# Kernel tuning notes

Measured on AMD Instinct MI355X. Metric: run time of the kernel, lower is better.

The kernel has to match this reference:

```python
import jax, jax.numpy as jnp
import numpy as np
import math

B, N, H = 2, 2048, 16
D_NOPE, D_ROPE, D_V = 128, 64, 128
Q_HEAD_DIM = D_NOPE + D_ROPE  # 192
HID, QR, KVR = 2048, 1536, 512
THETA = 10000.0
EPS = 1e-6


def _rmsnorm(x, w):
    var = jnp.mean(jnp.square(x.astype(jnp.float32)), axis=-1, keepdims=True)
    return w * (x * jax.lax.rsqrt(var + EPS)).astype(x.dtype)


def _permute_pairs(x):
    # torch: view(..., d//2, 2).transpose(-1,-2).reshape(..., d)
    # -> concat(evens, odds) along last dim
    return jnp.concatenate([x[..., 0::2], x[..., 1::2]], axis=-1)


def _rotate_half(x):
    x1, x2 = x[..., : x.shape[-1] // 2], x[..., x.shape[-1] // 2:]
    return jnp.concatenate([-x2, x1], axis=-1)


def _rope_tables(pos_ids):
    inv_freq = 1.0 / (THETA ** (jnp.arange(0, D_ROPE, 2, dtype=jnp.float32) / D_ROPE))
    t = jnp.arange(N, dtype=jnp.float32)
    freqs = jnp.outer(t, inv_freq)                 # [N, 32]
    emb = jnp.concatenate([freqs, freqs], axis=-1) # [N, 64]
    cos = jnp.cos(emb)[pos_ids][:, None]           # [B, 1, N, 64]
    sin = jnp.sin(emb)[pos_ids][:, None]
    return cos, sin


def mla_forward(x, Wq_down, q_norm_w, Wq_up, Wkv_down, kv_norm_w, Wkv_up, Wo, mask, pos_ids):
    b, n, _ = x.shape
    # low-rank Q path
    q = _rmsnorm(x @ Wq_down, q_norm_w) @ Wq_up          # [B, N, H*192]
    q = q.reshape(b, n, H, Q_HEAD_DIM).transpose(0, 2, 1, 3)  # [B, H, N, 192]
    q_nope, q_pe = q[..., :D_NOPE], q[..., D_NOPE:]
    # low-rank KV path
    kv = x @ Wkv_down                                    # [B, N, 512+64]
    kv_c, k_pe = kv[..., :KVR], kv[..., KVR:]
    k_pe = k_pe.reshape(b, n, 1, D_ROPE).transpose(0, 2, 1, 3)  # [B, 1, N, 64]
    kv_up = _rmsnorm(kv_c, kv_norm_w) @ Wkv_up           # [B, N, H*256]
    kv_up = kv_up.reshape(b, n, H, D_NOPE + D_V).transpose(0, 2, 1, 3)  # [B, H, N, 256]
    k_nope, v = kv_up[..., :D_NOPE], kv_up[..., D_NOPE:]
    # partial RoPE (with the pair-permute quirk from the torch code)
    cos, sin = _rope_tables(pos_ids)
    q_pe = _permute_pairs(q_pe)
    k_pe = _permute_pairs(k_pe)
    q_pe = q_pe * cos + _rotate_half(q_pe) * sin
    k_pe = k_pe * cos + _rotate_half(k_pe) * sin
    q_full = jnp.concatenate([q_nope, q_pe], axis=-1)                       # [B, H, N, 192]
    k_full = jnp.concatenate([k_nope, jnp.broadcast_to(k_pe, (b, H, n, D_ROPE))], axis=-1)
    scores = jnp.einsum('bhqd,bhkd->bhqk', q_full, k_full) / math.sqrt(Q_HEAD_DIM)
    scores = jnp.where(mask == 0, -jnp.inf, scores)
    attn = jax.nn.softmax(scores.astype(jnp.float32), axis=-1)
    out = jnp.einsum('bhqk,bhkd->bhqd', attn, v)          # [B, H, N, 128]
    out = out.transpose(0, 2, 1, 3).reshape(b, n, H * D_V)
    return out @ Wo


def setup_inputs() -> dict:
    key = jax.random.key(0)
    ks = jax.random.split(key, 7)
    s = 0.02
    return {
        'x': jax.random.normal(ks[0], (B, N, HID), jnp.float32),
        'Wq_down': jax.random.normal(ks[1], (HID, QR), jnp.float32) * s,
        'q_norm_w': jnp.ones((QR,), jnp.float32),
        'Wq_up': jax.random.normal(ks[2], (QR, H * Q_HEAD_DIM), jnp.float32) * s,
        'Wkv_down': jax.random.normal(ks[3], (HID, KVR + D_ROPE), jnp.float32) * s,
        'kv_norm_w': jnp.ones((KVR,), jnp.float32),
        'Wkv_up': jax.random.normal(ks[4], (KVR, H * (D_NOPE + D_V)), jnp.float32) * s,
        'Wo': jax.random.normal(ks[5], (H * D_V, HID), jnp.float32) * s,
        'mask': jnp.ones((1, 1, N, N), jnp.bool_),
        'pos_ids': jnp.broadcast_to(jnp.arange(N, dtype=jnp.int32), (B, N)),
    }


def reference(x, Wq_down, q_norm_w, Wq_up, Wkv_down, kv_norm_w, Wkv_up, Wo, mask, pos_ids):
    return mla_forward(x, Wq_down, q_norm_w, Wq_up, Wkv_down, kv_norm_w, Wkv_up, Wo, mask, pos_ids)
```

## Files before the change

kernel.cpp:

```cpp
#include <hip/hip_runtime.h>
#include <hip/hip_bf16.h>
#include <cstdint>

#define B_ 2
#define N_ 2048
#define H_ 16
#define HID_ 2048
#define QR_ 1536
#define KVR_ 512
#define DN_ 128
#define DR_ 64
#define DV_ 128
#define QHD_ 192

typedef __attribute__((ext_vector_type(8))) short short8;
typedef __attribute__((ext_vector_type(4))) float f32x4;

union bfu { __hip_bfloat16 b; short s; };

static __device__ __forceinline__ void bf_split(float v, short& hi, short& lo) {
  bfu uh, ul;
  uh.b = __float2bfloat16(v);
  float hf = __bfloat162float(uh.b);
  ul.b = __float2bfloat16(v - hf);
  hi = uh.s; lo = ul.s;
}

static __device__ __forceinline__ void gload16(const void* g, void* l) {
  __builtin_amdgcn_global_load_lds(
      (const __attribute__((address_space(1))) uint32_t*)(g),
      (__attribute__((address_space(3))) uint32_t*)(l), 16, 0, 0);
}


__global__ __launch_bounds__(256) void conv_a_kernel(
    const float* __restrict__ A, uint8_t* __restrict__ img, int K, int nks, int total) {
  int gid = blockIdx.x * 256 + threadIdx.x;
  if (gid >= total) return;
  int perRow = K >> 3;
  int row = gid / perRow, kc = (gid - row * perRow) << 3;
  const float* src = A + (size_t)row * K + kc;
  short8 hi, lo;
#pragma unroll
  for (int j = 0; j < 8; ++j) { short a, b; bf_split(src[j], a, b); hi[j] = a; lo[j] = b; }
  int mb = row >> 7, r = row & 127, sw = (r & 7) << 4;
  uint8_t* base = img + ((size_t)mb * nks << 14) + r * 128;
  auto put = [&](int p, short8 v) {
    int ks = p >> 6, s = (p >> 3) & 7;
    *(short8*)(base + ((size_t)ks << 14) + ((16 * s) ^ sw)) = v;
  };
  put(kc, hi); put(K + kc, lo); put(2 * K + kc, hi);
}

__global__ __launch_bounds__(256) void conv_b_kernel(
    const float* __restrict__ Bw, uint8_t* __restrict__ img, int K, int N,
    int Npad, int nbase, int nks, int total) {
  int gid = blockIdx.x * 256 + threadIdx.x;
  if (gid >= total) return;
  int perN = K >> 3;
  int n = gid / perN, kc = (gid - n * perN) << 3;
  short8 hi = {0,0,0,0,0,0,0,0}, lo = {0,0,0,0,0,0,0,0};
  if (n < N) {
#pragma unroll
    for (int j = 0; j < 8; ++j) {
      short a, b; bf_split(Bw[(size_t)(kc + j) * N + n], a, b); hi[j] = a; lo[j] = b;
    }
  }
  int nn = nbase * 128 + n;
  int nb = nn >> 7, r = nn & 127, sw = (r & 7) << 4;
  uint8_t* base = img + ((size_t)nb * nks << 14) + r * 128;
  auto put = [&](int p, short8 v) {
    int ks = p >> 6, s = (p >> 3) & 7;
    *(short8*)(base + ((size_t)ks << 14) + ((16 * s) ^ sw)) = v;
  };
  put(kc, hi); put(K + kc, hi); put(2 * K + kc, lo);
}

__global__ __launch_bounds__(256) void rmsnorm_img_kernel(
    const float* __restrict__ in, const float* __restrict__ w,
    uint8_t* __restrict__ img, int len, int istride, int nks) {
  __shared__ float red[4];
  const int row = blockIdx.x;
  const float* x = in + (size_t)row * istride;
  float ss = 0.f;
  for (int i = threadIdx.x; i < len; i += 256) { float v = x[i]; ss += v * v; }
#pragma unroll
  for (int o = 32; o > 0; o >>= 1) ss += __shfl_down(ss, o, 64);
  if ((threadIdx.x & 63) == 0) red[threadIdx.x >> 6] = ss;
  __syncthreads();
  if (threadIdx.x == 0)
    red[0] = rsqrtf((red[0] + red[1] + red[2] + red[3]) / (float)len + 1e-6f);
  __syncthreads();
  const float inv = red[0];
  int mb = row >> 7, r = row & 127, sw = (r & 7) << 4;
  uint8_t* base = img + ((size_t)mb * nks << 14) + r * 128;
  auto put = [&](int p, short8 v) {
    int ks = p >> 6, s = (p >> 3) & 7;
    *(short8*)(base + ((size_t)ks << 14) + ((16 * s) ^ sw)) = v;
  };
  for (int kc = threadIdx.x * 8; kc < len; kc += 2048) {
    short8 hi, lo;
#pragma unroll
    for (int j = 0; j < 8; ++j) {
      short a, b; bf_split(w[kc + j] * (x[kc + j] * inv), a, b); hi[j] = a; lo[j] = b;
    }
    put(kc, hi); put(len + kc, lo); put(2 * len + kc, hi);
  }
}

template <int MODE>
__global__ __launch_bounds__(256) void gemm_bf16_kernel(
    const uint8_t* __restrict__ Aimg, const uint8_t* __restrict__ Bimg,
    float* __restrict__ C, int N, int nks,
    uint8_t* __restrict__ Kn, uint8_t* __restrict__ Vv) {
  __shared__ __align__(16) uint8_t As[16384];
  __shared__ __align__(16) uint8_t Bs[16384];
  const int tid = threadIdx.x;
  const int lane = tid & 63;
  const int wave = tid >> 6;
  const int wm = wave >> 1, wn = wave & 1;
  const int lr = lane & 15, g = lane >> 4;
  const int mb = blockIdx.y, nb = blockIdx.x;
  const uint8_t* ga = Aimg + ((size_t)mb * nks << 14);
  const uint8_t* gb = Bimg + ((size_t)nb * nks << 14);

  f32x4 acc[4][4];
#pragma unroll
  for (int i = 0; i < 4; ++i)
#pragma unroll
    for (int j = 0; j < 4; ++j) acc[i][j] = (f32x4){0.f, 0.f, 0.f, 0.f};

  for (int ks = 0; ks < nks; ++ks) {
    __syncthreads();
#pragma unroll
    for (int i = 0; i < 4; ++i)
      gload16(ga + ((size_t)ks << 14) + (wave * 4 + i) * 1024 + lane * 16,
              As + (wave * 4 + i) * 1024);
#pragma unroll
    for (int i = 0; i < 4; ++i)
      gload16(gb + ((size_t)ks << 14) + (wave * 4 + i) * 1024 + lane * 16,
              Bs + (wave * 4 + i) * 1024);
    __syncthreads();
#pragma unroll
    for (int c = 0; c < 2; ++c) {
      short8 af[4], bf[4];
#pragma unroll
      for (int i = 0; i < 4; ++i) {
        int ar = wm * 64 + i * 16 + lr;
        af[i] = *(const short8*)(As + ar * 128 + ((16 * (c * 4 + g)) ^ ((ar & 7) << 4)));
        int br = wn * 64 + i * 16 + lr;
        bf[i] = *(const short8*)(Bs + br * 128 + ((16 * (c * 4 + g)) ^ ((br & 7) << 4)));
      }
#pragma unroll
      for (int i = 0; i < 4; ++i)
#pragma unroll
        for (int j = 0; j < 4; ++j)
          acc[i][j] = __builtin_amdgcn_mfma_f32_16x16x32_bf16(af[i], bf[j], acc[i][j], 0, 0, 0);
    }
  }

  if (MODE == 0) {
#pragma unroll
    for (int i = 0; i < 4; ++i)
#pragma unroll
      for (int q = 0; q < 4; ++q) {
        float* rp = C + (size_t)(mb * 128 + wm * 64 + i * 16 + g * 4 + q) * N +
                    nb * 128 + wn * 64 + lr;
#pragma unroll
        for (int j = 0; j < 4; ++j) rp[j * 16] = acc[i][j][q];
      }
  } else {
#pragma unroll
    for (int i = 0; i < 4; ++i)
#pragma unroll
      for (int j = 0; j < 4; ++j)
#pragma unroll
        for (int q = 0; q < 4; ++q) {
          int trow = mb * 128 + wm * 64 + i * 16 + g * 4 + q;
          int nn = nb * 128 + wn * 64 + j * 16 + lr;
          int h = nn >> 8, half = (nn >> 7) & 1, d = nn & 127;
          int b = trow >> 11, t = trow & 2047, kt = t >> 5, r = t & 31;
          int bh = b * 16 + h;
          short hi, lo; bf_split(acc[i][j][q], hi, lo);
          if (half == 0) {
            uint8_t* tp = Kn + (((size_t)bh * 64 + kt) << 14) + r * 512;
            int sw = (r & 7) << 4, s = d >> 3;
            *(short*)(tp + ((16 * s) ^ sw) + (d & 7) * 2) = hi;
            *(short*)(tp + ((16 * (s + 16)) ^ sw) + (d & 7) * 2) = lo;
          } else {
            uint8_t* tp = Vv + (((size_t)bh * 64 + kt) << 14) + d * 128;
            int sw = (d & 7) << 4, gg = r >> 3;
            *(short*)(tp + ((16 * gg) ^ sw) + (r & 7) * 2) = hi;
            *(short*)(tp + ((16 * (gg + 4)) ^ sw) + (r & 7) * 2) = lo;
          }
        }
  }
}

__device__ __forceinline__ void rope_apply(const float* __restrict__ src,
                                           float* __restrict__ dst, float pos) {
  float xv[64];
#pragma unroll
  for (int i = 0; i < 64; ++i) xv[i] = src[i];
#pragma unroll
  for (int i = 0; i < 32; ++i) {
    float freq = __expf(-0.2878231366f * (float)i);
    float s, c;
    sincosf(pos * freq, &s, &c);
    dst[i]      = xv[2 * i] * c - xv[2 * i + 1] * s;
    dst[i + 32] = xv[2 * i + 1] * c + xv[2 * i] * s;
  }
}

__global__ __launch_bounds__(256) void rope_q_kernel(float* __restrict__ q,
                                                     const int* __restrict__ pos_ids) {
  int idx = blockIdx.x * 256 + threadIdx.x;
  if (idx >= B_ * N_ * H_) return;
  int t = idx >> 4, h = idx & 15;
  float* p = q + (size_t)t * (H_ * QHD_) + h * QHD_ + DN_;
  rope_apply(p, p, (float)pos_ids[t]);
}

__global__ __launch_bounds__(256) void rope_k_kernel(const float* __restrict__ Cmat,
                                                     const int* __restrict__ pos_ids,
                                                     uint8_t* __restrict__ Kp) {
  int t = blockIdx.x * 256 + threadIdx.x;
  if (t >= B_ * N_) return;
  float rv[64];
  rope_apply(Cmat + (size_t)t * 2176 + 2048, rv, (float)pos_ids[t]);
  int b = t >> 11, tt = t & 2047, kt = tt >> 5, r = tt & 31;
  uint8_t* tp = Kp + (((size_t)b * 64 + kt) << 13) + r * 256;
  int sw = (r & 7) << 4;
#pragma unroll
  for (int s = 0; s < 8; ++s) {
    short8 hi, lo;
#pragma unroll
    for (int j = 0; j < 8; ++j) { short a, bq; bf_split(rv[s * 8 + j], a, bq); hi[j] = a; lo[j] = bq; }
    *(short8*)(tp + ((16 * s) ^ sw)) = hi;
    *(short8*)(tp + ((16 * (s + 8)) ^ sw)) = lo;
  }
}

__global__ __launch_bounds__(256, 3) void attn_mfma_kernel(
    const float* __restrict__ q_up,
    const uint8_t* __restrict__ Kn, const uint8_t* __restrict__ Kp,
    const uint8_t* __restrict__ Vv,
    float* __restrict__ aout) {
  __shared__ __align__(16) uint8_t Ksn[32 * 512];
  __shared__ __align__(16) uint8_t Ksp[32 * 256];
  __shared__ __align__(16) uint8_t Vs[128 * 128];
  __shared__ __align__(16) uint8_t Ps[4 * 2048];

  const int tid = threadIdx.x;
  const int lane = tid & 63;
  const int wave = tid >> 6;
  const int g = lane >> 4;
  const int lr = lane & 15;
  const int bh = blockIdx.y;
  const int b = bh >> 4, h = bh & 15;
  const int q0 = blockIdx.x << 6;

  short8 qhi[6], qlo[6];
  {
    const int tok = b * N_ + q0 + wave * 16 + lr;
    const float* qp = q_up + (size_t)tok * (H_ * QHD_) + h * QHD_;
    const float scale = 0.07216878364870323f;
#pragma unroll
    for (int c = 0; c < 6; ++c) {
      const float* src = qp + c * 32 + g * 8;
#pragma unroll
      for (int j = 0; j < 8; ++j) {
        short a, bq; bf_split(src[j] * scale, a, bq);
        qhi[c][j] = a; qlo[c][j] = bq;
      }
    }
  }

  f32x4 acc_o[8];
#pragma unroll
  for (int i = 0; i < 8; ++i) acc_o[i] = (f32x4){0.f, 0.f, 0.f, 0.f};
  float m_r[4], l_r[4];
#pragma unroll
  for (int j = 0; j < 4; ++j) { m_r[j] = -1e30f; l_r[j] = 0.f; }

  for (int kt = 0; kt < N_ / 32; ++kt) {
    __syncthreads();
    {
      const uint8_t* gkn = Kn + (((size_t)bh * 64 + kt) << 14);
      const uint8_t* gkp = Kp + (((size_t)b * 64 + kt) << 13);
      const uint8_t* gv  = Vv + (((size_t)bh * 64 + kt) << 14);
#pragma unroll
      for (int i = 0; i < 4; ++i)
        gload16(gkn + (wave * 4 + i) * 1024 + lane * 16, Ksn + (wave * 4 + i) * 1024);
#pragma unroll
      for (int i = 0; i < 2; ++i)
        gload16(gkp + (wave * 2 + i) * 1024 + lane * 16, Ksp + (wave * 2 + i) * 1024);
#pragma unroll
      for (int i = 0; i < 4; ++i)
        gload16(gv + (wave * 4 + i) * 1024 + lane * 16, Vs + (wave * 4 + i) * 1024);
    }
    __syncthreads();

    f32x4 accs[2];
#pragma unroll
    for (int t = 0; t < 2; ++t) {
      f32x4 a = {0.f, 0.f, 0.f, 0.f};
      const int krow = t * 16 + lr;
      const int sw = (krow & 7) << 4;
      const uint8_t* kb = Ksn + krow * 512;
#pragma unroll
      for (int c = 0; c < 4; ++c) {
        short8 kh = *(const short8*)(kb + ((16 * (c * 4 + g)) ^ sw));
        short8 kl = *(const short8*)(kb + ((16 * (c * 4 + g + 16)) ^ sw));
        a = __builtin_amdgcn_mfma_f32_16x16x32_bf16(qhi[c], kh, a, 0, 0, 0);
        a = __builtin_amdgcn_mfma_f32_16x16x32_bf16(qhi[c], kl, a, 0, 0, 0);
        a = __builtin_amdgcn_mfma_f32_16x16x32_bf16(qlo[c], kh, a, 0, 0, 0);
      }
      const uint8_t* pb = Ksp + krow * 256;
#pragma unroll
      for (int c2 = 0; c2 < 2; ++c2) {
        short8 kh = *(const short8*)(pb + ((16 * (c2 * 4 + g)) ^ sw));
        short8 kl = *(const short8*)(pb + ((16 * (c2 * 4 + g + 8)) ^ sw));
        a = __builtin_amdgcn_mfma_f32_16x16x32_bf16(qhi[4 + c2], kh, a, 0, 0, 0);
        a = __builtin_amdgcn_mfma_f32_16x16x32_bf16(qhi[4 + c2], kl, a, 0, 0, 0);
        a = __builtin_amdgcn_mfma_f32_16x16x32_bf16(qlo[4 + c2], kh, a, 0, 0, 0);
      }
      accs[t] = a;
    }

    float fac[4], p0[4], p1[4];
#pragma unroll
    for (int j = 0; j < 4; ++j) {
      float rm = fmaxf(accs[0][j], accs[1][j]);
      rm = fmaxf(rm, __shfl_xor(rm, 1, 64));
      rm = fmaxf(rm, __shfl_xor(rm, 2, 64));
      rm = fmaxf(rm, __shfl_xor(rm, 4, 64));
      rm = fmaxf(rm, __shfl_xor(rm, 8, 64));
      float mn = fmaxf(m_r[j], rm);
      fac[j] = __expf(m_r[j] - mn);
      m_r[j] = mn;
      p0[j] = __expf(accs[0][j] - mn);
      p1[j] = __expf(accs[1][j] - mn);
      float rs = p0[j] + p1[j];
      rs += __shfl_xor(rs, 1, 64);
      rs += __shfl_xor(rs, 2, 64);
      rs += __shfl_xor(rs, 4, 64);
      rs += __shfl_xor(rs, 8, 64);
      l_r[j] = l_r[j] * fac[j] + rs;
    }
#pragma unroll
    for (int dt = 0; dt < 8; ++dt) {
#pragma unroll
      for (int j = 0; j < 4; ++j) acc_o[dt][j] *= fac[j];
    }

    {
      uint8_t* pw = Ps + wave * 2048;
#pragma unroll
      for (int j = 0; j < 4; ++j) {
        int r = g * 4 + j;
        int rsw = (r & 7) << 4;
        uint8_t* rowp = pw + r * 128;
#pragma unroll
        for (int t = 0; t < 2; ++t) {
          float p = t ? p1[j] : p0[j];
          int k = t * 16 + lr;
          short a, bq; bf_split(p, a, bq);
          *(short*)(rowp + ((((k >> 3) + 0) * 16) ^ rsw) + (k & 7) * 2) = a;
          *(short*)(rowp + ((((k >> 3) + 4) * 16) ^ rsw) + (k & 7) * 2) = bq;
        }
      }
    }

    {
      const uint8_t* pr = Ps + wave * 2048 + lr * 128;
      const int psw = (lr & 7) << 4;
      short8 ph = *(const short8*)(pr + ((16 * g) ^ psw));
      short8 pl = *(const short8*)(pr + ((16 * (4 + g)) ^ psw));
#pragma unroll
      for (int dt = 0; dt < 8; ++dt) {
        int dcol = dt * 16 + lr;
        const uint8_t* vb = Vs + dcol * 128;
        int vsw = (dcol & 7) << 4;
        short8 vh = *(const short8*)(vb + ((16 * g) ^ vsw));
        short8 vl = *(const short8*)(vb + ((16 * (4 + g)) ^ vsw));
        acc_o[dt] = __builtin_amdgcn_mfma_f32_16x16x32_bf16(ph, vh, acc_o[dt], 0, 0, 0);
        acc_o[dt] = __builtin_amdgcn_mfma_f32_16x16x32_bf16(ph, vl, acc_o[dt], 0, 0, 0);
        acc_o[dt] = __builtin_amdgcn_mfma_f32_16x16x32_bf16(pl, vh, acc_o[dt], 0, 0, 0);
      }
    }
  }

  float inv[4];
#pragma unroll
  for (int j = 0; j < 4; ++j) inv[j] = 1.f / l_r[j];
  const int tokb = b * N_ + q0 + wave * 16 + g * 4;
#pragma unroll
  for (int j = 0; j < 4; ++j) {
    float* orow = aout + (size_t)(tokb + j) * (H_ * DV_) + h * DV_;
#pragma unroll
    for (int dt = 0; dt < 8; ++dt)
      orow[dt * 16 + lr] = acc_o[dt][j] * inv[j];
  }
}

extern "C" void kernel_launch(void* const* d_in, const int* in_sizes, int n_in,
                              void* d_out, int out_size, void* d_ws, size_t ws_size,
                              hipStream_t stream) {
  (void)in_sizes; (void)n_in; (void)out_size; (void)ws_size;
  const float* x         = (const float*)d_in[0];
  const float* Wq_down   = (const float*)d_in[1];
  const float* q_norm_w  = (const float*)d_in[2];
  const float* Wq_up     = (const float*)d_in[3];
  const float* Wkv_down  = (const float*)d_in[4];
  const float* kv_norm_w = (const float*)d_in[5];
  const float* Wkv_up    = (const float*)d_in[6];
  const float* Wo        = (const float*)d_in[7];
  const int* pos_ids     = (const int*)d_in[9];
  float* out = (float*)d_out;

  uint8_t* W = (uint8_t*)d_ws;
  uint8_t* Aimg  = W;
  uint8_t* Bimg  = W + 50331648;
  float*   q_up  = (float*)(W + 78643200);
  float*   qtkv  = (float*)(W + 128974848);
  uint8_t* Knimg = W + 128974848;
  uint8_t* Kpimg = W + 164626432;
  float*   a_out = (float*)(W + 0);
  uint8_t* Aimg2 = W + 50331648;
  uint8_t* Woimg = W + 100663296;
  uint8_t* Vimg  = (uint8_t*)d_out;

  dim3 blk(256);
  conv_a_kernel<<<4096, blk, 0, stream>>>(x, Aimg, 2048, 96, 4096 * 256);
  conv_b_kernel<<<1536, blk, 0, stream>>>(Wq_down, Bimg, 2048, 1536, 1536, 0, 96, 1536 * 256);
  conv_b_kernel<<<640, blk, 0, stream>>>(Wkv_down, Bimg, 2048, 576, 640, 12, 96, 640 * 256);
  gemm_bf16_kernel<0><<<dim3(17, 32), blk, 0, stream>>>(Aimg, Bimg, qtkv, 2176, 96, nullptr, nullptr);
  rmsnorm_img_kernel<<<4096, blk, 0, stream>>>(qtkv, q_norm_w, Aimg, 1536, 2176, 72);
  conv_b_kernel<<<2304, blk, 0, stream>>>(Wq_up, Bimg, 1536, 3072, 3072, 0, 72, 2304 * 256);
  gemm_bf16_kernel<0><<<dim3(24, 32), blk, 0, stream>>>(Aimg, Bimg, q_up, 3072, 72, nullptr, nullptr);
  rope_q_kernel<<<256, blk, 0, stream>>>(q_up, pos_ids);
  rope_k_kernel<<<16, blk, 0, stream>>>(qtkv, pos_ids, Kpimg);
  rmsnorm_img_kernel<<<4096, blk, 0, stream>>>(qtkv + 1536, kv_norm_w, Aimg, 512, 2176, 24);
  conv_b_kernel<<<1024, blk, 0, stream>>>(Wkv_up, Bimg, 512, 4096, 4096, 0, 24, 1024 * 256);
  gemm_bf16_kernel<1><<<dim3(32, 32), blk, 0, stream>>>(Aimg, Bimg, nullptr, 4096, 24, Knimg, Vimg);
  attn_mfma_kernel<<<dim3(32, 32), blk, 0, stream>>>(q_up, Knimg, Kpimg, Vimg, a_out);
  conv_a_kernel<<<4096, blk, 0, stream>>>(a_out, Aimg2, 2048, 96, 4096 * 256);
  conv_b_kernel<<<2048, blk, 0, stream>>>(Wo, Woimg, 2048, 2048, 2048, 0, 96, 2048 * 256);
  gemm_bf16_kernel<0><<<dim3(16, 32), blk, 0, stream>>>(Aimg2, Woimg, out, 2048, 96, nullptr, nullptr);
}
```

Measured before the change: 1.221 ms.

## Double query rows per attention wave and split KV epilogue into conversion kernels

The attention kernel now handles 128 queries per block, two 16-row tiles per wave, so each K/V tile loaded into shared memory feeds twice as many MFMAs. This halves the number of K/V reloads per head. Occupancy drops to 2 blocks per CU, with more registers and a doubled P buffer. The scattered 2-byte hi/lo stores in the KV-up GEMM epilogue are replaced by a plain fp32 store plus two separate conversion kernels that write the swizzled K and V images with vector stores. This adds an extra fp32 round trip through memory and re-plans the workspace layout.

```diff
diff --git a/kernel.cpp b/kernel.cpp
--- a/kernel.cpp
+++ b/kernel.cpp
@@ -108,11 +108,9 @@
   }
 }
 
-template <int MODE>
 __global__ __launch_bounds__(256) void gemm_bf16_kernel(
     const uint8_t* __restrict__ Aimg, const uint8_t* __restrict__ Bimg,
-    float* __restrict__ C, int N, int nks,
-    uint8_t* __restrict__ Kn, uint8_t* __restrict__ Vv) {
+    float* __restrict__ C, int N, int nks) {
   __shared__ __align__(16) uint8_t As[16384];
   __shared__ __align__(16) uint8_t Bs[16384];
   const int tid = threadIdx.x;
@@ -158,42 +156,53 @@
           acc[i][j] = __builtin_amdgcn_mfma_f32_16x16x32_bf16(af[i], bf[j], acc[i][j], 0, 0, 0);
     }
   }
-
-  if (MODE == 0) {
-#pragma unroll
-    for (int i = 0; i < 4; ++i)
-#pragma unroll
-      for (int q = 0; q < 4; ++q) {
-        float* rp = C + (size_t)(mb * 128 + wm * 64 + i * 16 + g * 4 + q) * N +
-                    nb * 128 + wn * 64 + lr;
-#pragma unroll
-        for (int j = 0; j < 4; ++j) rp[j * 16] = acc[i][j][q];
-      }
-  } else {
-#pragma unroll
-    for (int i = 0; i < 4; ++i)
-#pragma unroll
-      for (int j = 0; j < 4; ++j)
-#pragma unroll
-        for (int q = 0; q < 4; ++q) {
-          int trow = mb * 128 + wm * 64 + i * 16 + g * 4 + q;
-          int nn = nb * 128 + wn * 64 + j * 16 + lr;
-          int h = nn >> 8, half = (nn >> 7) & 1, d = nn & 127;
-          int b = trow >> 11, t = trow & 2047, kt = t >> 5, r = t & 31;
-          int bh = b * 16 + h;
-          short hi, lo; bf_split(acc[i][j][q], hi, lo);
-          if (half == 0) {
-            uint8_t* tp = Kn + (((size_t)bh * 64 + kt) << 14) + r * 512;
-            int sw = (r & 7) << 4, s = d >> 3;
-            *(short*)(tp + ((16 * s) ^ sw) + (d & 7) * 2) = hi;
-            *(short*)(tp + ((16 * (s + 16)) ^ sw) + (d & 7) * 2) = lo;
-          } else {
-            uint8_t* tp = Vv + (((size_t)bh * 64 + kt) << 14) + d * 128;
-            int sw = (d & 7) << 4, gg = r >> 3;
-            *(short*)(tp + ((16 * gg) ^ sw) + (r & 7) * 2) = hi;
-            *(short*)(tp + ((16 * (gg + 4)) ^ sw) + (r & 7) * 2) = lo;
-          }
-        }
+#pragma unroll
+  for (int i = 0; i < 4; ++i)
+#pragma unroll
+    for (int q = 0; q < 4; ++q) {
+      float* rp = C + (size_t)(mb * 128 + wm * 64 + i * 16 + g * 4 + q) * N +
+                  nb * 128 + wn * 64 + lr;
+#pragma unroll
+      for (int j = 0; j < 4; ++j) rp[j * 16] = acc[i][j][q];
+    }
+}
+
+__global__ __launch_bounds__(256) void conv_kn_kernel(
+    const float* __restrict__ kv_up, uint8_t* __restrict__ Kn) {
+  const int kt = blockIdx.x, bh = blockIdx.y;
+  const int b = bh >> 4, h = bh & 15;
+  uint8_t* tile = Kn + (((size_t)bh * 64 + kt) << 14);
+  for (int f = threadIdx.x; f < 512; f += 256) {
+    int r = f >> 4, s = f & 15;
+    int tok = b * N_ + kt * 32 + r;
+    const float* src = kv_up + (size_t)tok * 4096 + h * 256 + s * 8;
+    short8 hi, lo;
+#pragma unroll
+    for (int j = 0; j < 8; ++j) { short a, bq; bf_split(src[j], a, bq); hi[j] = a; lo[j] = bq; }
+    int sw = (r & 7) << 4;
+    *(short8*)(tile + r * 512 + ((16 * s) ^ sw)) = hi;
+    *(short8*)(tile + r * 512 + ((16 * (s + 16)) ^ sw)) = lo;
+  }
+}
+
+__global__ __launch_bounds__(256) void conv_v_kernel(
+    const float* __restrict__ kv_up, uint8_t* __restrict__ Vimg) {
+  const int kt = blockIdx.x, bh = blockIdx.y;
+  const int b = bh >> 4, h = bh & 15;
+  uint8_t* tile = Vimg + (((size_t)bh * 64 + kt) << 14);
+  for (int f = threadIdx.x; f < 512; f += 256) {
+    int d = f >> 2, gg = f & 3;
+    int tok0 = b * N_ + kt * 32 + gg * 8;
+    short8 hi, lo;
+#pragma unroll
+    for (int j = 0; j < 8; ++j) {
+      short a, bq;
+      bf_split(kv_up[(size_t)(tok0 + j) * 4096 + h * 256 + 128 + d], a, bq);
+      hi[j] = a; lo[j] = bq;
+    }
+    int sw = (d & 7) << 4;
+    *(short8*)(tile + d * 128 + ((16 * gg) ^ sw)) = hi;
+    *(short8*)(tile + d * 128 + ((16 * (4 + gg)) ^ sw)) = lo;
   }
 }
 
@@ -241,7 +250,7 @@
   }
 }
 
-__global__ __launch_bounds__(256, 3) void attn_mfma_kernel(
+__global__ __launch_bounds__(256, 2) void attn_mfma_kernel(
     const float* __restrict__ q_up,
     const uint8_t* __restrict__ Kn, const uint8_t* __restrict__ Kp,
     const uint8_t* __restrict__ Vv,
@@ -249,7 +258,7 @@
   __shared__ __align__(16) uint8_t Ksn[32 * 512];
   __shared__ __align__(16) uint8_t Ksp[32 * 256];
   __shared__ __align__(16) uint8_t Vs[128 * 128];
-  __shared__ __align__(16) uint8_t Ps[4 * 2048];
+  __shared__ __align__(16) uint8_t Ps[4 * 4096];
 
   const int tid = threadIdx.x;
   const int lane = tid & 63;
@@ -258,30 +267,37 @@
   const int lr = lane & 15;
   const int bh = blockIdx.y;
   const int b = bh >> 4, h = bh & 15;
-  const int q0 = blockIdx.x << 6;
-
-  short8 qhi[6], qlo[6];
+  const int q0 = blockIdx.x << 7;
+
+  short8 qhi[2][6], qlo[2][6];
   {
-    const int tok = b * N_ + q0 + wave * 16 + lr;
-    const float* qp = q_up + (size_t)tok * (H_ * QHD_) + h * QHD_;
     const float scale = 0.07216878364870323f;
 #pragma unroll
-    for (int c = 0; c < 6; ++c) {
-      const float* src = qp + c * 32 + g * 8;
-#pragma unroll
-      for (int j = 0; j < 8; ++j) {
-        short a, bq; bf_split(src[j] * scale, a, bq);
-        qhi[c][j] = a; qlo[c][j] = bq;
-      }
-    }
-  }
-
-  f32x4 acc_o[8];
-#pragma unroll
-  for (int i = 0; i < 8; ++i) acc_o[i] = (f32x4){0.f, 0.f, 0.f, 0.f};
-  float m_r[4], l_r[4];
-#pragma unroll
-  for (int j = 0; j < 4; ++j) { m_r[j] = -1e30f; l_r[j] = 0.f; }
+    for (int tl = 0; tl < 2; ++tl) {
+      const int tok = b * N_ + q0 + wave * 32 + tl * 16 + lr;
+      const float* qp = q_up + (size_t)tok * (H_ * QHD_) + h * QHD_;
+#pragma unroll
+      for (int c = 0; c < 6; ++c) {
+        const float* src = qp + c * 32 + g * 8;
+#pragma unroll
+        for (int j = 0; j < 8; ++j) {
+          short a, bq; bf_split(src[j] * scale, a, bq);
+          qhi[tl][c][j] = a; qlo[tl][c][j] = bq;
+        }
+      }
+    }
+  }
+
+  f32x4 acc_o[2][8];
+#pragma unroll
+  for (int tl = 0; tl < 2; ++tl)
+#pragma unroll
+    for (int i = 0; i < 8; ++i) acc_o[tl][i] = (f32x4){0.f, 0.f, 0.f, 0.f};
+  float m_r[2][4], l_r[2][4];
+#pragma unroll
+  for (int tl = 0; tl < 2; ++tl)
+#pragma unroll
+    for (int j = 0; j < 4; ++j) { m_r[tl][j] = -1e30f; l_r[tl][j] = 0.f; }
 
   for (int kt = 0; kt < N_ / 32; ++kt) {
     __syncthreads();
@@ -301,10 +317,11 @@
     }
     __syncthreads();
 
-    f32x4 accs[2];
+    f32x4 accs[2][2];
 #pragma unroll
     for (int t = 0; t < 2; ++t) {
-      f32x4 a = {0.f, 0.f, 0.f, 0.f};
+      f32x4 aA = {0.f, 0.f, 0.f, 0.f};
+      f32x4 aB = {0.f, 0.f, 0.f, 0.f};
       const int krow = t * 16 + lr;
       const int sw = (krow & 7) << 4;
       const uint8_t* kb = Ksn + krow * 512;
@@ -312,50 +329,60 @@
       for (int c = 0; c < 4; ++c) {
         short8 kh = *(const short8*)(kb + ((16 * (c * 4 + g)) ^ sw));
         short8 kl = *(const short8*)(kb + ((16 * (c * 4 + g + 16)) ^ sw));
-        a = __builtin_amdgcn_mfma_f32_16x16x32_bf16(qhi[c], kh, a, 0, 0, 0);
-        a = __builtin_amdgcn_mfma_f32_16x16x32_bf16(qhi[c], kl, a, 0, 0, 0);
-        a = __builtin_amdgcn_mfma_f32_16x16x32_bf16(qlo[c], kh, a, 0, 0, 0);
+        aA = __builtin_amdgcn_mfma_f32_16x16x32_bf16(qhi[0][c], kh, aA, 0, 0, 0);
+        aA = __builtin_amdgcn_mfma_f32_16x16x32_bf16(qhi[0][c], kl, aA, 0, 0, 0);
+        aA = __builtin_amdgcn_mfma_f32_16x16x32_bf16(qlo[0][c], kh, aA, 0, 0, 0);
+        aB = __builtin_amdgcn_mfma_f32_16x16x32_bf16(qhi[1][c], kh, aB, 0, 0, 0);
+        aB = __builtin_amdgcn_mfma_f32_16x16x32_bf16(qhi[1][c], kl, aB, 0, 0, 0);
+        aB = __builtin_amdgcn_mfma_f32_16x16x32_bf16(qlo[1][c], kh, aB, 0, 0, 0);
       }
       const uint8_t* pb = Ksp + krow * 256;
 #pragma unroll
       for (int c2 = 0; c2 < 2; ++c2) {
         short8 kh = *(const short8*)(pb + ((16 * (c2 * 4 + g)) ^ sw));
         short8 kl = *(const short8*)(pb + ((16 * (c2 * 4 + g + 8)) ^ sw));
-        a = __builtin_amdgcn_mfma_f32_16x16x32_bf16(qhi[4 + c2], kh, a, 0, 0, 0);
-        a = __builtin_amdgcn_mfma_f32_16x16x32_bf16(qhi[4 + c2], kl, a, 0, 0, 0);
-        a = __builtin_amdgcn_mfma_f32_16x16x32_bf16(qlo[4 + c2], kh, a, 0, 0, 0);
-      }
-      accs[t] = a;
-    }
-
-    float fac[4], p0[4], p1[4];
-#pragma unroll
-    for (int j = 0; j < 4; ++j) {
-      float rm = fmaxf(accs[0][j], accs[1][j]);
-      rm = fmaxf(rm, __shfl_xor(rm, 1, 64));
-      rm = fmaxf(rm, __shfl_xor(rm, 2, 64));
-      rm = fmaxf(rm, __shfl_xor(rm, 4, 64));
-      rm = fmaxf(rm, __shfl_xor(rm, 8, 64));
-      float mn = fmaxf(m_r[j], rm);
-      fac[j] = __expf(m_r[j] - mn);
-      m_r[j] = mn;
-      p0[j] = __expf(accs[0][j] - mn);
-      p1[j] = __expf(accs[1][j] - mn);
-      float rs = p0[j] + p1[j];
-      rs += __shfl_xor(rs, 1, 64);
-      rs += __shfl_xor(rs, 2, 64);
-      rs += __shfl_xor(rs, 4, 64);
-      rs += __shfl_xor(rs, 8, 64);
-      l_r[j] = l_r[j] * fac[j] + rs;
-    }
-#pragma unroll
-    for (int dt = 0; dt < 8; ++dt) {
-#pragma unroll
-      for (int j = 0; j < 4; ++j) acc_o[dt][j] *= fac[j];
-    }
-
-    {
-      uint8_t* pw = Ps + wave * 2048;
+        aA = __builtin_amdgcn_mfma_f32_16x16x32_bf16(qhi[0][4 + c2], kh, aA, 0, 0, 0);
+        aA = __builtin_amdgcn_mfma_f32_16x16x32_bf16(qhi[0][4 + c2], kl, aA, 0, 0, 0);
+        aA = __builtin_amdgcn_mfma_f32_16x16x32_bf16(qlo[0][4 + c2], kh, aA, 0, 0, 0);
+        aB = __builtin_amdgcn_mfma_f32_16x16x32_bf16(qhi[1][4 + c2], kh, aB, 0, 0, 0);
+        aB = __builtin_amdgcn_mfma_f32_16x16x32_bf16(qhi[1][4 + c2], kl, aB, 0, 0, 0);
+        aB = __builtin_amdgcn_mfma_f32_16x16x32_bf16(qlo[1][4 + c2], kh, aB, 0, 0, 0);
+      }
+      accs[0][t] = aA; accs[1][t] = aB;
+    }
+
+    float fac[2][4], p0[2][4], p1[2][4];
+#pragma unroll
+    for (int tl = 0; tl < 2; ++tl)
+#pragma unroll
+      for (int j = 0; j < 4; ++j) {
+        float rm = fmaxf(accs[tl][0][j], accs[tl][1][j]);
+        rm = fmaxf(rm, __shfl_xor(rm, 1, 64));
+        rm = fmaxf(rm, __shfl_xor(rm, 2, 64));
+        rm = fmaxf(rm, __shfl_xor(rm, 4, 64));
+        rm = fmaxf(rm, __shfl_xor(rm, 8, 64));
+        float mn = fmaxf(m_r[tl][j], rm);
+        fac[tl][j] = __expf(m_r[tl][j] - mn);
+        m_r[tl][j] = mn;
+        p0[tl][j] = __expf(accs[tl][0][j] - mn);
+        p1[tl][j] = __expf(accs[tl][1][j] - mn);
+        float rs = p0[tl][j] + p1[tl][j];
+        rs += __shfl_xor(rs, 1, 64);
+        rs += __shfl_xor(rs, 2, 64);
+        rs += __shfl_xor(rs, 4, 64);
+        rs += __shfl_xor(rs, 8, 64);
+        l_r[tl][j] = l_r[tl][j] * fac[tl][j] + rs;
+      }
+#pragma unroll
+    for (int tl = 0; tl < 2; ++tl)
+#pragma unroll
+      for (int dt = 0; dt < 8; ++dt)
+#pragma unroll
+        for (int j = 0; j < 4; ++j) acc_o[tl][dt][j] *= fac[tl][j];
+
+#pragma unroll
+    for (int tl = 0; tl < 2; ++tl) {
+      uint8_t* pw = Ps + wave * 4096 + tl * 2048;
 #pragma unroll
       for (int j = 0; j < 4; ++j) {
         int r = g * 4 + j;
@@ -363,7 +390,7 @@
         uint8_t* rowp = pw + r * 128;
 #pragma unroll
         for (int t = 0; t < 2; ++t) {
-          float p = t ? p1[j] : p0[j];
+          float p = t ? p1[tl][j] : p0[tl][j];
           int k = t * 16 + lr;
           short a, bq; bf_split(p, a, bq);
           *(short*)(rowp + ((((k >> 3) + 0) * 16) ^ rsw) + (k & 7) * 2) = a;
@@ -373,10 +400,13 @@
     }
 
     {
-      const uint8_t* pr = Ps + wave * 2048 + lr * 128;
+      const uint8_t* prA = Ps + wave * 4096 + lr * 128;
+      const uint8_t* prB = prA + 2048;
       const int psw = (lr & 7) << 4;
-      short8 ph = *(const short8*)(pr + ((16 * g) ^ psw));
-      short8 pl = *(const short8*)(pr + ((16 * (4 + g)) ^ psw));
+      short8 phA = *(const short8*)(prA + ((16 * g) ^ psw));
+      short8 plA = *(const short8*)(prA + ((16 * (4 + g)) ^ psw));
+      short8 phB = *(const short8*)(prB + ((16 * g) ^ psw));
+      short8 plB = *(const short8*)(prB + ((16 * (4 + g)) ^ psw));
 #pragma unroll
       for (int dt = 0; dt < 8; ++dt) {
         int dcol = dt * 16 + lr;
@@ -384,23 +414,29 @@
         int vsw = (dcol & 7) << 4;
         short8 vh = *(const short8*)(vb + ((16 * g) ^ vsw));
         short8 vl = *(const short8*)(vb + ((16 * (4 + g)) ^ vsw));
-        acc_o[dt] = __builtin_amdgcn_mfma_f32_16x16x32_bf16(ph, vh, acc_o[dt], 0, 0, 0);
-        acc_o[dt] = __builtin_amdgcn_mfma_f32_16x16x32_bf16(ph, vl, acc_o[dt], 0, 0, 0);
-        acc_o[dt] = __builtin_amdgcn_mfma_f32_16x16x32_bf16(pl, vh, acc_o[dt], 0, 0, 0);
-      }
-    }
-  }
-
-  float inv[4];
-#pragma unroll
-  for (int j = 0; j < 4; ++j) inv[j] = 1.f / l_r[j];
-  const int tokb = b * N_ + q0 + wave * 16 + g * 4;
-#pragma unroll
-  for (int j = 0; j < 4; ++j) {
-    float* orow = aout + (size_t)(tokb + j) * (H_ * DV_) + h * DV_;
-#pragma unroll
-    for (int dt = 0; dt < 8; ++dt)
-      orow[dt * 16 + lr] = acc_o[dt][j] * inv[j];
+        acc_o[0][dt] = __builtin_amdgcn_mfma_f32_16x16x32_bf16(phA, vh, acc_o[0][dt], 0, 0, 0);
+        acc_o[0][dt] = __builtin_amdgcn_mfma_f32_16x16x32_bf16(phA, vl, acc_o[0][dt], 0, 0, 0);
+        acc_o[0][dt] = __builtin_amdgcn_mfma_f32_16x16x32_bf16(plA, vh, acc_o[0][dt], 0, 0, 0);
+        acc_o[1][dt] = __builtin_amdgcn_mfma_f32_16x16x32_bf16(phB, vh, acc_o[1][dt], 0, 0, 0);
+        acc_o[1][dt] = __builtin_amdgcn_mfma_f32_16x16x32_bf16(phB, vl, acc_o[1][dt], 0, 0, 0);
+        acc_o[1][dt] = __builtin_amdgcn_mfma_f32_16x16x32_bf16(plB, vh, acc_o[1][dt], 0, 0, 0);
+      }
+    }
+  }
+
+#pragma unroll
+  for (int tl = 0; tl < 2; ++tl) {
+    float inv[4];
+#pragma unroll
+    for (int j = 0; j < 4; ++j) inv[j] = 1.f / l_r[tl][j];
+    const int tokb = b * N_ + q0 + wave * 32 + tl * 16 + g * 4;
+#pragma unroll
+    for (int j = 0; j < 4; ++j) {
+      float* orow = aout + (size_t)(tokb + j) * (H_ * DV_) + h * DV_;
+#pragma unroll
+      for (int dt = 0; dt < 8; ++dt)
+        orow[dt * 16 + lr] = acc_o[tl][dt][j] * inv[j];
+    }
   }
 }
 
@@ -420,32 +456,37 @@
   float* out = (float*)d_out;
 
   uint8_t* W = (uint8_t*)d_ws;
-  uint8_t* Aimg  = W;
-  uint8_t* Bimg  = W + 50331648;
-  float*   q_up  = (float*)(W + 78643200);
-  float*   qtkv  = (float*)(W + 128974848);
-  uint8_t* Knimg = W + 128974848;
-  uint8_t* Kpimg = W + 164626432;
+  uint8_t* Xi    = W;
+  uint8_t* Bslot = W + 50331648;
+  float*   qtkv  = (float*)(W + 79691776);
+  float*   q_up  = (float*)(W + 115343360);
+  uint8_t* Kpimg = W + 165675008;
+  uint8_t* KvAimg= W + 67108864;
+  uint8_t* WkvBimg=W + 79691776;
+  float*   kv_up = (float*)(W + 0);
+  uint8_t* Knimg = W + 67108864;
   float*   a_out = (float*)(W + 0);
-  uint8_t* Aimg2 = W + 50331648;
+  uint8_t* A2img = W + 33554432;
   uint8_t* Woimg = W + 100663296;
   uint8_t* Vimg  = (uint8_t*)d_out;
 
   dim3 blk(256);
-  conv_a_kernel<<<4096, blk, 0, stream>>>(x, Aimg, 2048, 96, 4096 * 256);
-  conv_b_kernel<<<1536, blk, 0, stream>>>(Wq_down, Bimg, 2048, 1536, 1536, 0, 96, 1536 * 256);
-  conv_b_kernel<<<640, blk, 0, stream>>>(Wkv_down, Bimg, 2048, 576, 640, 12, 96, 640 * 256);
-  gemm_bf16_kernel<0><<<dim3(17, 32), blk, 0, stream>>>(Aimg, Bimg, qtkv, 2176, 96, nullptr, nullptr);
-  rmsnorm_img_kernel<<<4096, blk, 0, stream>>>(qtkv, q_norm_w, Aimg, 1536, 2176, 72);
-  conv_b_kernel<<<2304, blk, 0, stream>>>(Wq_up, Bimg, 1536, 3072, 3072, 0, 72, 2304 * 256);
-  gemm_bf16_kernel<0><<<dim3(24, 32), blk, 0, stream>>>(Aimg, Bimg, q_up, 3072, 72, nullptr, nullptr);
+  conv_a_kernel<<<4096, blk, 0, stream>>>(x, Xi, 2048, 96, 4096 * 256);
+  conv_b_kernel<<<1536, blk, 0, stream>>>(Wq_down, Bslot, 2048, 1536, 1536, 0, 96, 1536 * 256);
+  conv_b_kernel<<<640, blk, 0, stream>>>(Wkv_down, Bslot, 2048, 576, 640, 12, 96, 640 * 256);
+  gemm_bf16_kernel<<<dim3(17, 32), blk, 0, stream>>>(Xi, Bslot, qtkv, 2176, 96);
+  rmsnorm_img_kernel<<<4096, blk, 0, stream>>>(qtkv, q_norm_w, Xi, 1536, 2176, 72);
+  conv_b_kernel<<<2304, blk, 0, stream>>>(Wq_up, Bslot, 1536, 3072, 3072, 0, 72, 2304 * 256);
+  gemm_bf16_kernel<<<dim3(24, 32), blk, 0, stream>>>(Xi, Bslot, q_up, 3072, 72);
   rope_q_kernel<<<256, blk, 0, stream>>>(q_up, pos_ids);
   rope_k_kernel<<<16, blk, 0, stream>>>(qtkv, pos_ids, Kpimg);
-  rmsnorm_img_kernel<<<4096, blk, 0, stream>>>(qtkv + 1536, kv_norm_w, Aimg, 512, 2176, 24);
-  conv_b_kernel<<<1024, blk, 0, stream>>>(Wkv_up, Bimg, 512, 4096, 4096, 0, 24, 1024 * 256);
-  gemm_bf16_kernel<1><<<dim3(32, 32), blk, 0, stream>>>(Aimg, Bimg, nullptr, 4096, 24, Knimg, Vimg);
-  attn_mfma_kernel<<<dim3(32, 32), blk, 0, stream>>>(q_up, Knimg, Kpimg, Vimg, a_out);
-  conv_a_kernel<<<4096, blk, 0, stream>>>(a_out, Aimg2, 2048, 96, 4096 * 256);
+  rmsnorm_img_kernel<<<4096, blk, 0, stream>>>(qtkv + 1536, kv_norm_w, KvAimg, 512, 2176, 24);
+  conv_b_kernel<<<1024, blk, 0, stream>>>(Wkv_up, WkvBimg, 512, 4096, 4096, 0, 24, 1024 * 256);
+  gemm_bf16_kernel<<<dim3(32, 32), blk, 0, stream>>>(KvAimg, WkvBimg, kv_up, 4096, 24);
+  conv_kn_kernel<<<dim3(64, 32), blk, 0, stream>>>(kv_up, Knimg);
+  conv_v_kernel<<<dim3(64, 32), blk, 0, stream>>>(kv_up, Vimg);
+  attn_mfma_kernel<<<dim3(16, 32), blk, 0, stream>>>(q_up, Knimg, Kpimg, Vimg, a_out);
+  conv_a_kernel<<<4096, blk, 0, stream>>>(a_out, A2img, 2048, 96, 4096 * 256);
   conv_b_kernel<<<2048, blk, 0, stream>>>(Wo, Woimg, 2048, 2048, 2048, 0, 96, 2048 * 256);
-  gemm_bf16_kernel<0><<<dim3(16, 32), blk, 0, stream>>>(Aimg2, Woimg, out, 2048, 96, nullptr, nullptr);
-}
+  gemm_bf16_kernel<<<dim3(16, 32), blk, 0, stream>>>(A2img, Woimg, out, 2048, 96);
+}
```

Measured after the change: 1.169 ms. 1.04x faster.
